# Kernel optimization log

Hardware: AMD Instinct MI355X
Metric: run time of the kernel (lower is better)

Reference implementation:

```python
import jax, jax.numpy as jnp
import numpy as np

NUM_GROUP, GROUP_SIZE = 128, 32
MASK = (64, 32, 32)
FEAT_DIM, N_POINTS = 1024, 2048
NBR_K = int(1.2 * GROUP_SIZE)  # int(nbr_ratio * group_size) = 38
SUPPORT, NBHD = 8, 32
W_RECON, W_MATCH, W_LATENT, W_MAN = 1.0, 1.0, 1.0, 0.1

gather = jax.vmap(lambda p, i: p[i])  # batched index_points

def sqdist(a, b):  # [B,M,3],[B,N,3] -> [B,M,N]
    return (jnp.sum(a * a, -1)[:, :, None] + jnp.sum(b * b, -1)[:, None, :]
            - 2.0 * jnp.einsum('bmd,bnd->bmn', a, b))

def knn_idx(q, db, k):  # indices into db of k nearest to each query
    return jax.lax.top_k(-sqdist(q, db), k)[1]

def fps(pts, G):  # farthest point sampling, [B,N,3] -> [B,G] indices
    b, n, _ = pts.shape
    def step(carry, _):
        min_d, far = carry
        cur = jnp.take_along_axis(pts, far[:, None, None], axis=1)
        min_d = jnp.minimum(min_d, jnp.sum((pts - cur) ** 2, -1))
        return (min_d, jnp.argmax(min_d, -1).astype(jnp.int32)), far
    init = (jnp.full((b, n), 1e10, dtype=pts.dtype), jnp.zeros((b,), jnp.int32))
    _, idxs = jax.lax.scan(step, init, None, length=G)
    return idxs.T

def bn(h, g, b_, m, v):  # BatchNorm1d, eval-mode running stats
    return (h - m) * jax.lax.rsqrt(v + 1e-5) * g + b_

def chamfer_l1(a, b):
    d = sqdist(a, b)
    d1 = jnp.sqrt(jnp.maximum(jnp.min(d, axis=2), 1e-12))
    d2 = jnp.sqrt(jnp.maximum(jnp.min(d, axis=1), 1e-12))
    return 0.5 * (d1.mean() + d2.mean())

def estimate_normals(xyz, K):  # PCA normal per point + direction disambiguation
    nb = gather(xyz, knn_idx(xyz, xyz, K))          # [B,N,K,3]
    c = nb - nb.mean(axis=2, keepdims=True)
    cov = jnp.einsum('bnki,bnkj->bnij', c, c) / K   # [B,N,3,3]
    _, v = jnp.linalg.eigh(cov)
    n = v[..., 0]                                   # smallest-eigenvalue eigvec
    proj = jnp.einsum('bnkd,bnd->bn', nb - xyz[:, :, None, :], n)
    return n * jnp.where(proj >= 0.0, 1.0, -1.0)[..., None]

def forward_all(pts, W1, b1, g1, be1, m1, v1, W2, b2, W3, b3, g2, be2, m2, v2,
                W4, b4, D1W, D1b, D2W, D2b, D3W, D3b, D4W, D4b):
    bsz = pts.shape[0]
    def encoder(x):  # PCN encoder: pointwise convs + global max pooling
        n = x.shape[1]
        h = jax.nn.relu(bn(x @ W1.T + b1, g1, be1, m1, v1))
        h = h @ W2.T + b2                           # [B,n,256]
        gmax = h.max(axis=1)
        h = jnp.concatenate([jnp.broadcast_to(gmax[:, None, :], (bsz, n, gmax.shape[-1])), h], axis=-1)
        h = jax.nn.relu(bn(h @ W3.T + b3, g2, be2, m2, v2))
        return (h @ W4.T + b4).max(axis=1)          # [B,FEAT_DIM]
    def decoder(z):
        h = jax.nn.relu(z @ D1W.T + D1b)
        h = jax.nn.relu(h @ D2W.T + D2b)
        h = jax.nn.relu(h @ D3W.T + D3b)
        return (h @ D4W.T + D4b).reshape(bsz, -1, 3)
    # --- Group divider: FPS centers + knn neighborhoods (centered) ---
    center = gather(pts, fps(pts, NUM_GROUP))       # [B,G,3]
    nbrs = gather(pts, knn_idx(center, pts, GROUP_SIZE)) - center[:, :, None, :]
    o1, o2 = MASK[0], MASK[0] + MASK[1]             # identity perm partition
    ng = (nbrs[:, :o1], nbrs[:, o1:o2], nbrs[:, o2:])
    cg = (center[:, :o1], center[:, o1:o2], center[:, o2:])
    rebuild0 = (ng[0] + cg[0][:, :, None, :]).reshape(bsz, -1, 3)
    feat = encoder(rebuild0)
    pred = decoder(feat)                            # [B,N_POINTS,3]
    # shape reconstruction loss
    idx = knn_idx(cg[0], pred, NBR_K)
    l_recon = W_RECON * chamfer_l1(rebuild0, gather(pred, idx).reshape(bsz, -1, 3))
    # shape matching loss
    rebuild1 = (ng[1] + cg[1][:, :, None, :]).reshape(bsz, -1, 3)
    idx = knn_idx(cg[1], pred, NBR_K)
    l_match = W_MATCH * chamfer_l1(rebuild1, gather(pred, idx).reshape(bsz, -1, 3))
    # latent reconstruction (detached input) - SmoothL1
    idx = knn_idx(cg[2], pred, GROUP_SIZE)
    feat_recon = encoder(jax.lax.stop_gradient(gather(pred, idx).reshape(bsz, -1, 3)))
    diff = feat - feat_recon
    ad = jnp.abs(diff)
    l_latent = W_LATENT * jnp.where(ad < 1.0, 0.5 * diff * diff, ad - 0.5).mean()
    # manifoldness (normal consistency) constraint
    normals = estimate_normals(pred, NBHD)
    nb = gather(normals, knn_idx(pred, pred, SUPPORT))  # [B,N,8,3]
    a = nb[:, :, :1, :]
    cos = jnp.sum(a * nb, -1) / (jnp.maximum(jnp.linalg.norm(a, axis=-1), 1e-6)
                                 * jnp.maximum(jnp.linalg.norm(nb, axis=-1), 1e-6))
    l_man = W_MAN * jnp.std(1.0 - cos, axis=-1, ddof=1).mean(axis=-1).mean()
    total = l_recon + l_match + l_latent + l_man
    return total, l_recon, l_match, l_latent, l_man


def setup_inputs() -> dict:
    ks = jax.random.split(jax.random.key(0), 10)
    rn = lambda k, sh: jax.random.normal(k, sh, jnp.float32) * 0.02
    z, o = jnp.zeros, jnp.ones
    return dict(
        pts=jax.random.normal(ks[0], (16, 2048, 3), jnp.float32),
        W1=rn(ks[1], (128, 3)), b1=z(128), g1=o(128), be1=z(128), m1=z(128), v1=o(128),
        W2=rn(ks[2], (256, 128)), b2=z(256),
        W3=rn(ks[3], (512, 512)), b3=z(512), g2=o(512), be2=z(512), m2=z(512), v2=o(512),
        W4=rn(ks[4], (FEAT_DIM, 512)), b4=z(FEAT_DIM),
        D1W=rn(ks[5], (2048, FEAT_DIM)), D1b=z(2048),
        D2W=rn(ks[6], (2048, 2048)), D2b=z(2048),
        D3W=rn(ks[7], (2048, 2048)), D3b=z(2048),
        D4W=rn(ks[8], (3 * N_POINTS, 2048)), D4b=z(3 * N_POINTS),
    )


def reference(pts, W1, b1, g1, be1, m1, v1, W2, b2, W3, b3, g2, be2, m2, v2,
              W4, b4, D1W, D1b, D2W, D2b, D3W, D3b, D4W, D4b):
    return forward_all(pts, W1, b1, g1, be1, m1, v1, W2, b2, W3, b3, g2, be2,
                       m2, v2, W4, b4, D1W, D1b, D2W, D2b, D3W, D3b, D4W, D4b)
```

## Files before the change

### kernel.cpp

```cpp
#include <hip/hip_runtime.h>
#include <math.h>

#define BSZ 16
#define NPTS 2048
#define NG 128
#define GS 32
#define NBRK 38

typedef _Float16 f16;
typedef _Float16 f16x8 __attribute__((ext_vector_type(8)));
typedef float f32x4 __attribute__((ext_vector_type(4)));

__device__ __forceinline__ unsigned fkey(float x) {
    unsigned u = __float_as_uint(x);
    return (u >> 31) ? ~u : (u | 0x80000000u);
}
__device__ __forceinline__ float fkey_inv(unsigned k) {
    unsigned u = (k >> 31) ? (k ^ 0x80000000u) : ~k;
    return __uint_as_float(u);
}

__device__ __forceinline__ unsigned wave_min_u32(unsigned v) {
    unsigned t;
    t = (unsigned)__builtin_amdgcn_update_dpp(-1, (int)v, 0x111, 0xF, 0xF, false);
    v = v < t ? v : t;
    t = (unsigned)__builtin_amdgcn_update_dpp(-1, (int)v, 0x112, 0xF, 0xF, false);
    v = v < t ? v : t;
    t = (unsigned)__builtin_amdgcn_update_dpp(-1, (int)v, 0x114, 0xF, 0xF, false);
    v = v < t ? v : t;
    t = (unsigned)__builtin_amdgcn_update_dpp(-1, (int)v, 0x118, 0xF, 0xF, false);
    v = v < t ? v : t;
    t = (unsigned)__builtin_amdgcn_update_dpp(-1, (int)v, 0x142, 0xA, 0xF, false);
    v = v < t ? v : t;
    t = (unsigned)__builtin_amdgcn_update_dpp(-1, (int)v, 0x143, 0xC, 0xF, false);
    v = v < t ? v : t;
    return (unsigned)__builtin_amdgcn_readlane((int)v, 63);
}

__device__ __forceinline__ unsigned long long wave_max_u64(unsigned long long v) {
#define DPPSTEP(ctrl, rmask)                                                                \
    {                                                                                       \
        unsigned tlo = (unsigned)__builtin_amdgcn_update_dpp(0, (int)(unsigned)v, ctrl,     \
                                                             rmask, 0xF, false);            \
        unsigned thi = (unsigned)__builtin_amdgcn_update_dpp(0, (int)(unsigned)(v >> 32),   \
                                                             ctrl, rmask, 0xF, false);      \
        unsigned long long t = ((unsigned long long)thi << 32) | tlo;                       \
        v = t > v ? t : v;                                                                  \
    }
    DPPSTEP(0x111, 0xF)
    DPPSTEP(0x112, 0xF)
    DPPSTEP(0x114, 0xF)
    DPPSTEP(0x118, 0xF)
    DPPSTEP(0x142, 0xA)
    DPPSTEP(0x143, 0xC)
#undef DPPSTEP
    unsigned rlo = (unsigned)__builtin_amdgcn_readlane((int)(unsigned)v, 63);
    unsigned rhi = (unsigned)__builtin_amdgcn_readlane((int)(unsigned)(v >> 32), 63);
    return ((unsigned long long)rhi << 32) | rlo;
}

__global__ __launch_bounds__(256, 1) void fps_kernel_v5(const float* __restrict__ pts,
                                                        f32x4* __restrict__ center4) {
    int b = blockIdx.x;
    const float* P = pts + (size_t)b * NPTS * 3;
    int tid = threadIdx.x;
    int lane = tid & 63, wave = tid >> 6;
    __shared__ __align__(16) float Pl[NPTS * 3];
    __shared__ __align__(16) float slot[2][4][8];
#pragma unroll
    for (int i = 0; i < 6; ++i) {
        int v4 = tid + i * 256;
        ((f32x4*)Pl)[v4] = ((const f32x4*)P)[v4];
    }
    __syncthreads();
    float px[8], py[8], pz[8], mind[8];
#pragma unroll
    for (int m = 0; m < 8; ++m) {
        int j = tid + (m << 8);
        px[m] = Pl[j * 3 + 0];
        py[m] = Pl[j * 3 + 1];
        pz[m] = Pl[j * 3 + 2];
        mind[m] = 1e10f;
    }
    float cx = Pl[0], cy = Pl[1], cz = Pl[2];
    f32x4* C4 = center4 + (size_t)b * NG;
#pragma unroll 1
    for (int g = 0; g < NG; ++g) {
        if (tid == 0) C4[g] = (f32x4){cx, cy, cz, cx * cx + cy * cy + cz * cz};
        if (g == NG - 1) break;
        float best0 = -1.f, best1 = -1.f;
        int bm0 = 0, bm1 = 1;
#pragma unroll
        for (int m = 0; m < 8; m += 2) {
            float dx0 = px[m] - cx, dy0 = py[m] - cy, dz0 = pz[m] - cz;
            float d0 = dx0 * dx0 + dy0 * dy0 + dz0 * dz0;
            float md0 = fminf(mind[m], d0);
            mind[m] = md0;
            if (md0 > best0) { best0 = md0; bm0 = m; }
            float dx1 = px[m + 1] - cx, dy1 = py[m + 1] - cy, dz1 = pz[m + 1] - cz;
            float d1 = dx1 * dx1 + dy1 * dy1 + dz1 * dz1;
            float md1 = fminf(mind[m + 1], d1);
            mind[m + 1] = md1;
            if (md1 > best1) { best1 = md1; bm1 = m + 1; }
        }
        bool t = (best1 > best0) || (best1 == best0 && bm1 < bm0);
        float bv = t ? best1 : best0;
        int bi = t ? bm1 : bm0;
        unsigned j = (unsigned)(tid + (bi << 8));
        unsigned long long key =
            ((unsigned long long)__float_as_uint(bv) << 32) | (unsigned)(~j);
        key = wave_max_u64(key);
        unsigned bj = ~(unsigned)key;
        int par = g & 1;
        if (lane < 3) slot[par][wave][2 + lane] = Pl[bj * 3 + lane];
        if (lane == 0) {
            slot[par][wave][0] = __uint_as_float((unsigned)key);
            slot[par][wave][1] = __uint_as_float((unsigned)(key >> 32));
        }
        __syncthreads();
        unsigned long long kb = 0ull;
        float nx = 0.f, ny = 0.f, nz = 0.f;
#pragma unroll
        for (int w = 0; w < 4; ++w) {
            f32x4 v = *(const f32x4*)&slot[par][w][0];
            float vz = slot[par][w][4];
            unsigned long long kk =
                ((unsigned long long)__float_as_uint(v[1]) << 32) | __float_as_uint(v[0]);
            bool tw = kk > kb;
            kb = tw ? kk : kb;
            nx = tw ? v[2] : nx;
            ny = tw ? v[3] : ny;
            nz = tw ? vz : nz;
        }
        cx = nx; cy = ny; cz = nz;
    }
}

__device__ __forceinline__ void knn_query_p4(f32x4 q, const f32x4* __restrict__ db4,
                                             int k, int* __restrict__ o, int lane) {
    const unsigned KINF = 0xFFFFFFFFu;
    float m2x = -2.f * q[0], m2y = -2.f * q[1], m2z = -2.f * q[2], qq = q[3];
    unsigned key[32];
    unsigned c0 = KINF, c1 = KINF, c2 = KINF, c3 = KINF;
#pragma unroll
    for (int m = 0; m < 32; ++m) {
        int j = lane + (m << 6);
        f32x4 b = db4[j];
        float t = fmaf(m2x, b[0], b[3]);
        t = fmaf(m2y, b[1], t);
        t = fmaf(m2z, b[2], t);
        float dv = qq + t;
        unsigned qd = (unsigned)fminf(fmaxf(dv, 0.f) * 8192.0f, 2097151.f);
        unsigned kk = (qd << 11) | (unsigned)j;
        key[m] = kk;
        if (kk < c3) {
            if (kk < c2) {
                c3 = c2;
                if (kk < c1) {
                    c2 = c1;
                    if (kk < c0) { c1 = c0; c0 = kk; } else c1 = kk;
                } else c2 = kk;
            } else c3 = kk;
        }
    }
    unsigned hw = c3;
    int ncached = 4;
    for (int r = 0; r < k; ++r) {
        bool need = (c0 == KINF) && (ncached < 32);
        if (__any(need)) {
            unsigned best = KINF;
#pragma unroll
            for (int m = 0; m < 32; ++m) {
                unsigned v = key[m];
                best = (v > hw && v < best) ? v : best;
            }
            if (need) {
                c0 = best;
                hw = best;
                ncached = (best == KINF) ? 32 : ncached + 1;
            }
        }
        unsigned g = wave_min_u32(c0);
        if (lane == 0) o[r] = (int)(g & 0x7FFu);
        if (((g & 0x7FFu) & 63u) == (unsigned)lane) {
            c0 = c1; c1 = c2; c2 = c3; c3 = KINF;
        }
    }
}

__global__ void knn_group_kernel(const f32x4* __restrict__ center4,
                                 const f32x4* __restrict__ pts4,
                                 int* __restrict__ knnc) {
    int wave = threadIdx.x >> 6, lane = threadIdx.x & 63;
    int qidx = blockIdx.x * 4 + wave;
    int b = qidx >> 7, qi = qidx & 127;
    knn_query_p4(center4[(size_t)b * NG + qi], pts4 + (size_t)b * NPTS, GS,
                 knnc + (size_t)qidx * GS, lane);
}

__global__ void knn_post_kernel(const f32x4* __restrict__ center4,
                                const f32x4* __restrict__ pred4,
                                int* __restrict__ idxa, int* __restrict__ idxb,
                                int* __restrict__ idxc, int* __restrict__ knn32) {
    int wave = threadIdx.x >> 6, lane = threadIdx.x & 63;
    if (blockIdx.x < 512) {
        int qidx = blockIdx.x * 4 + wave;
        int b = qidx >> 7, qi = qidx & 127;
        const f32x4* db4 = pred4 + (size_t)b * NPTS;
        int k; int* o;
        if (qi < 64) { k = NBRK; o = idxa + ((size_t)b * 64 + qi) * NBRK; }
        else if (qi < 96) { k = NBRK; o = idxb + ((size_t)b * 32 + qi - 64) * NBRK; }
        else { k = GS; o = idxc + ((size_t)b * 32 + qi - 96) * GS; }
        knn_query_p4(center4[(size_t)b * NG + qi], db4, k, o, lane);
    } else {
        int qidx = (blockIdx.x - 512) * 4 + wave;
        int b = qidx >> 11, qi = qidx & 2047;
        const f32x4* db4 = pred4 + (size_t)b * NPTS;
        knn_query_p4(db4[qi], db4, GS, knn32 + (size_t)qidx * GS, lane);
    }
}

__global__ void gather_rebuild_kernel(const f32x4* __restrict__ pts4,
                                      const int* __restrict__ knnc,
                                      f32x4* __restrict__ r0p4,
                                      f32x4* __restrict__ r1p4) {
    int t = blockIdx.x * 256 + threadIdx.x;
    if (t < BSZ * 2048) {
        int b = t >> 11, j = t & 2047;
        int s = knnc[(size_t)b * (NG * GS) + j];
        r0p4[t] = pts4[(size_t)b * NPTS + s];
    } else {
        int tt = t - BSZ * 2048;
        int b = tt >> 10, j = tt & 1023;
        int s = knnc[(size_t)b * (NG * GS) + 2048 + j];
        r1p4[tt] = pts4[(size_t)b * NPTS + s];
    }
}

__global__ void gather_abc_kernel(const f32x4* __restrict__ pred4,
                                  const int* __restrict__ idxa,
                                  const int* __restrict__ idxb,
                                  const int* __restrict__ idxc,
                                  f32x4* __restrict__ gap4,
                                  f32x4* __restrict__ gbp4,
                                  f32x4* __restrict__ gathc4) {
    const int NA = BSZ * 2432, NB_ = BSZ * 1216, NC = BSZ * 1024;
    int t = blockIdx.x * 256 + threadIdx.x;
    if (t < NA) {
        int b = t / 2432, j = t - b * 2432;
        int s = idxa[(size_t)b * 2432 + j];
        gap4[t] = pred4[(size_t)b * NPTS + s];
    } else if (t < NA + NB_) {
        int tt = t - NA;
        int b = tt / 1216, j = tt - b * 1216;
        int s = idxb[(size_t)b * 1216 + j];
        gbp4[tt] = pred4[(size_t)b * NPTS + s];
    } else if (t < NA + NB_ + NC) {
        int tt = t - NA - NB_;
        int b = tt >> 10, j = tt & 1023;
        int s = idxc[(size_t)b * 1024 + j];
        gathc4[tt] = pred4[(size_t)b * NPTS + s];
    }
}

__global__ void cvt_all_kernel(const float* __restrict__ W2, const float* __restrict__ W3,
                               const float* __restrict__ W4, const float* __restrict__ pts,
                               f16* __restrict__ W2h, f16* __restrict__ W3h,
                               f16* __restrict__ W4h, f32x4* __restrict__ pts4) {
    int t = blockIdx.x * 256 + threadIdx.x;
    if (t < 32768) {
        int n = t >> 7, k = t & 127;
        W2h[t] = (f16)W2[(size_t)n * 128 + k];
    } else if (t < 163840) {
        int u = t - 32768;
        int n = u >> 8, k = u & 255;
        W3h[u] = (f16)W3[(size_t)n * 512 + 256 + k];
    } else if (t < 688128) {
        int u = t - 163840;
        int n = u >> 9, k = u & 511;
        W4h[u] = (f16)W4[(size_t)n * 512 + k];
    } else if (t < 688128 + BSZ * NPTS) {
        int u = t - 688128;
        float x = pts[(size_t)u * 3 + 0], y = pts[(size_t)u * 3 + 1],
              z = pts[(size_t)u * 3 + 2];
        pts4[u] = (f32x4){x, y, z, x * x + y * y + z * z};
    }
}

__global__ void pack_pred4_kernel(const float* __restrict__ pred,
                                  f32x4* __restrict__ pred4) {
    int t = blockIdx.x * 256 + threadIdx.x;
    if (t >= BSZ * NPTS) return;
    float x = pred[(size_t)t * 3 + 0], y = pred[(size_t)t * 3 + 1],
          z = pred[(size_t)t * 3 + 2];
    pred4[t] = (f32x4){x, y, z, x * x + y * y + z * z};
}

__global__ void layer1_kernel(const f32x4* __restrict__ X4, const float* __restrict__ W1,
                              const float* __restrict__ b1, const float* __restrict__ g1,
                              const float* __restrict__ be1, const float* __restrict__ m1,
                              const float* __restrict__ v1, f16* __restrict__ H1, int M) {
    __shared__ float w[384], bb[128], sg[128], sb[128], sm[128], sv[128];
    for (int i = threadIdx.x; i < 384; i += 256) w[i] = W1[i];
    if (threadIdx.x < 128) {
        int c = threadIdx.x;
        bb[c] = b1[c]; sg[c] = g1[c]; sb[c] = be1[c]; sm[c] = m1[c]; sv[c] = v1[c];
    }
    __syncthreads();
    int t = blockIdx.x * 256 + threadIdx.x;
    if (t >= M * 16) return;
    int row = t >> 4, cg = (t & 15) * 8;
    f32x4 xv = X4[row];
    float x0 = xv[0], x1 = xv[1], x2 = xv[2];
    f16x8 outv;
#pragma unroll
    for (int j = 0; j < 8; ++j) {
        int c = cg + j;
        float tv = x0 * w[c * 3] + x1 * w[c * 3 + 1] + x2 * w[c * 3 + 2] + bb[c];
        float vv = (tv - sm[c]) * rsqrtf(sv[c] + 1e-5f) * sg[c] + sb[c];
        outv[j] = (f16)fmaxf(vv, 0.f);
    }
    *(f16x8*)&H1[(size_t)row * 128 + cg] = outv;
}

__global__ __launch_bounds__(256) void mfma_gemm_kernel(
        const f16* __restrict__ A, const f16* __restrict__ W, int K, int N,
        const float* __restrict__ bias, const float* __restrict__ bias2d,
        const float* __restrict__ bng, const float* __restrict__ bnb,
        const float* __restrict__ bnm, const float* __restrict__ bnv,
        f16* __restrict__ Cout, unsigned* __restrict__ maxkey,
        int rows_per_batch, int relu) {
    __shared__ f16 Als[128 * 40];
    __shared__ f16 Bls[128 * 40];
    int tid = threadIdx.x;
    int lane = tid & 63;
    int wave = tid >> 6;
    int wm = wave & 1, wn = wave >> 1;
    int c16 = lane & 15, quad = lane >> 4;
    int gx = gridDim.x;
    int nwg = gx * gridDim.y;
    int lin = blockIdx.y * gx + blockIdx.x;
    int qc = nwg >> 3, rc = nwg & 7;
    int xcd = lin & 7, pos = lin >> 3;
    int nlin = (xcd < rc ? xcd * (qc + 1) : rc * (qc + 1) + (xcd - rc) * qc) + pos;
    int row0 = (nlin / gx) * 128, col0 = (nlin % gx) * 128;
    int sr = tid >> 2;
    int skc = (tid & 3) * 8;

    f32x4 acc[4][4];
#pragma unroll
    for (int i = 0; i < 4; ++i)
#pragma unroll
        for (int j = 0; j < 4; ++j) acc[i][j] = (f32x4){0.f, 0.f, 0.f, 0.f};

    const f16* Ab = A + (size_t)(row0 + sr) * K + skc;
    const f16* Ab2 = A + (size_t)(row0 + sr + 64) * K + skc;
    const f16* Wb = W + (size_t)(col0 + sr) * K + skc;
    const f16* Wb2 = W + (size_t)(col0 + sr + 64) * K + skc;

    f16x8 pa0 = *(const f16x8*)Ab;
    f16x8 pa1 = *(const f16x8*)Ab2;
    f16x8 pb0 = *(const f16x8*)Wb;
    f16x8 pb1 = *(const f16x8*)Wb2;

    for (int k0 = 0; k0 < K; k0 += 32) {
        *(f16x8*)&Als[sr * 40 + skc] = pa0;
        *(f16x8*)&Als[(sr + 64) * 40 + skc] = pa1;
        *(f16x8*)&Bls[sr * 40 + skc] = pb0;
        *(f16x8*)&Bls[(sr + 64) * 40 + skc] = pb1;
        __syncthreads();
        if (k0 + 32 < K) {
            int kn = k0 + 32;
            pa0 = *(const f16x8*)(Ab + kn);
            pa1 = *(const f16x8*)(Ab2 + kn);
            pb0 = *(const f16x8*)(Wb + kn);
            pb1 = *(const f16x8*)(Wb2 + kn);
        }
        f16x8 af[4], bf[4];
#pragma unroll
        for (int s = 0; s < 4; ++s) {
            af[s] = *(const f16x8*)&Als[(wm * 64 + s * 16 + c16) * 40 + quad * 8];
            bf[s] = *(const f16x8*)&Bls[(wn * 64 + s * 16 + c16) * 40 + quad * 8];
        }
#pragma unroll
        for (int ms = 0; ms < 4; ++ms)
#pragma unroll
            for (int ns = 0; ns < 4; ++ns)
                acc[ms][ns] = __builtin_amdgcn_mfma_f32_16x16x32_f16(af[ms], bf[ns],
                                                                     acc[ms][ns], 0, 0, 0);
        __syncthreads();
    }

    int b = row0 / rows_per_batch;
#pragma unroll
    for (int ns = 0; ns < 4; ++ns) {
        int col = col0 + wn * 64 + ns * 16 + c16;
        float bv = bias ? bias[col] : 0.f;
        float b2v = bias2d ? bias2d[(size_t)b * N + col] : 0.f;
        float mx = -3e38f;
#pragma unroll
        for (int ms = 0; ms < 4; ++ms) {
#pragma unroll
            for (int j = 0; j < 4; ++j) {
                float v = acc[ms][ns][j] + bv + b2v;
                if (bng) v = (v - bnm[col]) * rsqrtf(bnv[col] + 1e-5f) * bng[col] + bnb[col];
                if (relu) v = fmaxf(v, 0.f);
                if (Cout)
                    Cout[(size_t)(row0 + wm * 64 + ms * 16 + quad * 4 + j) * N + col] = (f16)v;
                mx = fmaxf(mx, v);
            }
        }
        if (maxkey) {
            mx = fmaxf(mx, __shfl_xor(mx, 16, 64));
            mx = fmaxf(mx, __shfl_xor(mx, 32, 64));
            if (quad == 0) atomicMax(&maxkey[(size_t)b * N + col], fkey(mx));
        }
    }
}

__global__ void skinny_v2_kernel(const float* __restrict__ A, const float* __restrict__ W,
                                 int ldw, int woff, const float* __restrict__ bias,
                                 float* __restrict__ C, int K, int N, int relu, int akey) {
    int wave = threadIdx.x >> 6, lane = threadIdx.x & 63;
    int col = blockIdx.x * 4 + wave;
    if (col >= N) return;
    const float* w = W + (size_t)col * ldw + woff;
    float acc[16];
#pragma unroll
    for (int m = 0; m < 16; ++m) acc[m] = 0.f;
    for (int k0 = 0; k0 < K; k0 += 256) {
        f32x4 wv = *(const f32x4*)(w + k0 + lane * 4);
#pragma unroll
        for (int m = 0; m < 16; ++m) {
            f32x4 av = *(const f32x4*)(A + (size_t)m * K + k0 + lane * 4);
            if (akey) {
#pragma unroll
                for (int u = 0; u < 4; ++u) av[u] = fkey_inv(__float_as_uint(av[u]));
            }
            acc[m] += av[0] * wv[0] + av[1] * wv[1] + av[2] * wv[2] + av[3] * wv[3];
        }
    }
#pragma unroll
    for (int m = 0; m < 16; ++m)
#pragma unroll
        for (int s = 1; s < 64; s <<= 1) acc[m] += __shfl_xor(acc[m], s, 64);
    if (lane == 0) {
        float bv = bias[col];
#pragma unroll
        for (int m = 0; m < 16; ++m) {
            float v = acc[m] + bv;
            if (relu) v = fmaxf(v, 0.f);
            C[(size_t)m * N + col] = v;
        }
    }
}

__global__ __launch_bounds__(256) void chamfer4_kernel(const f32x4* __restrict__ r0p4,
                                                       const f32x4* __restrict__ gap4,
                                                       const f32x4* __restrict__ r1p4,
                                                       const f32x4* __restrict__ gbp4,
                                                       float* __restrict__ accum) {
    __shared__ __align__(16) float Bl[2432 * 4];
    int blk = blockIdx.x;
    const f32x4 *A4, *B4; int na, nb, base, bpb; float* slot;
    if (blk < 128)      { A4 = r0p4; na = 2048; B4 = gap4; nb = 2432; slot = accum + 0; base = 0;   bpb = 8; }
    else if (blk < 288) { A4 = gap4; na = 2432; B4 = r0p4; nb = 2048; slot = accum + 1; base = 128; bpb = 10; }
    else if (blk < 352) { A4 = r1p4; na = 1024; B4 = gbp4; nb = 1216; slot = accum + 2; base = 288; bpb = 4; }
    else                { A4 = gbp4; na = 1216; B4 = r1p4; nb = 1024; slot = accum + 3; base = 352; bpb = 5; }
    int rel = blk - base;
    int b = rel / bpb, chunk = rel - b * bpb;
    for (int i = threadIdx.x; i < nb; i += 256)
        ((f32x4*)Bl)[i] = B4[(size_t)b * nb + i];
    __syncthreads();
    int aidx = chunk * 256 + threadIdx.x;
    float val = 0.f;
    if (aidx < na) {
        f32x4 a = A4[(size_t)b * na + aidx];
        float m2x = -2.f * a[0], m2y = -2.f * a[1], m2z = -2.f * a[2];
        float m0 = 3e38f, m1 = 3e38f, m2 = 3e38f, m3 = 3e38f;
        for (int j = 0; j < nb; j += 4) {
            f32x4 b0 = ((const f32x4*)Bl)[j + 0];
            f32x4 b1 = ((const f32x4*)Bl)[j + 1];
            f32x4 b2 = ((const f32x4*)Bl)[j + 2];
            f32x4 b3 = ((const f32x4*)Bl)[j + 3];
            float t0 = fmaf(m2z, b0[2], fmaf(m2y, b0[1], fmaf(m2x, b0[0], b0[3])));
            float t1 = fmaf(m2z, b1[2], fmaf(m2y, b1[1], fmaf(m2x, b1[0], b1[3])));
            float t2 = fmaf(m2z, b2[2], fmaf(m2y, b2[1], fmaf(m2x, b2[0], b2[3])));
            float t3 = fmaf(m2z, b3[2], fmaf(m2y, b3[1], fmaf(m2x, b3[0], b3[3])));
            m0 = fminf(m0, t0); m1 = fminf(m1, t1);
            m2 = fminf(m2, t2); m3 = fminf(m3, t3);
        }
        float m = fminf(fminf(m0, m1), fminf(m2, m3));
        val = sqrtf(fmaxf(a[3] + m, 1e-12f));
    }
    __shared__ float sdata[256];
    sdata[threadIdx.x] = val;
    __syncthreads();
    for (int s = 128; s > 0; s >>= 1) {
        if (threadIdx.x < s) sdata[threadIdx.x] += sdata[threadIdx.x + s];
        __syncthreads();
    }
    if (threadIdx.x == 0) atomicAdd(slot, sdata[0]);
}

__device__ void smallest_evec(double cxx, double cxy, double cxz,
                              double cyy, double cyz, double czz, double ev[3]) {
    double p1 = cxy * cxy + cxz * cxz + cyz * cyz;
    double q = (cxx + cyy + czz) / 3.0;
    double p2 = (cxx - q) * (cxx - q) + (cyy - q) * (cyy - q) + (czz - q) * (czz - q) + 2.0 * p1;
    double lam = q;
    if (p2 > 0.0) {
        double p = sqrt(p2 / 6.0);
        double b00 = (cxx - q) / p, b11 = (cyy - q) / p, b22 = (czz - q) / p;
        double b01 = cxy / p, b02 = cxz / p, b12 = cyz / p;
        double detB = b00 * (b11 * b22 - b12 * b12) - b01 * (b01 * b22 - b12 * b02)
                    + b02 * (b01 * b12 - b11 * b02);
        double r = detB * 0.5;
        r = r < -1.0 ? -1.0 : (r > 1.0 ? 1.0 : r);
        double phi = acos(r) / 3.0;
        lam = q + 2.0 * p * cos(phi + 2.0943951023931953);
    }
    double r0x = cxx - lam, r0y = cxy, r0z = cxz;
    double r1x = cxy, r1y = cyy - lam, r1z = cyz;
    double r2x = cxz, r2y = cyz, r2z = czz - lam;
    double c0x = r0y * r1z - r0z * r1y, c0y = r0z * r1x - r0x * r1z, c0z = r0x * r1y - r0y * r1x;
    double c1x = r0y * r2z - r0z * r2y, c1y = r0z * r2x - r0x * r2z, c1z = r0x * r2y - r0y * r2x;
    double c2x = r1y * r2z - r1z * r2y, c2y = r1z * r2x - r1x * r2z, c2z = r1x * r2y - r1y * r2x;
    double n0 = c0x * c0x + c0y * c0y + c0z * c0z;
    double n1 = c1x * c1x + c1y * c1y + c1z * c1z;
    double n2 = c2x * c2x + c2y * c2y + c2z * c2z;
    double bx = c0x, by = c0y, bz = c0z, bn = n0;
    if (n1 > bn) { bx = c1x; by = c1y; bz = c1z; bn = n1; }
    if (n2 > bn) { bx = c2x; by = c2y; bz = c2z; bn = n2; }
    if (bn < 1e-280) { ev[0] = 1.0; ev[1] = 0.0; ev[2] = 0.0; return; }
    double inv = 1.0 / sqrt(bn);
    ev[0] = bx * inv; ev[1] = by * inv; ev[2] = bz * inv;
}

__global__ __launch_bounds__(64) void normals_kernel(const f32x4* __restrict__ pred4,
                                                     const int* __restrict__ knn,
                                                     float* __restrict__ nrm) {
    int t = blockIdx.x * 64 + threadIdx.x;
    if (t >= BSZ * NPTS) return;
    int b = t / NPTS, i = t % NPTS;
    const f32x4* P4 = pred4 + (size_t)b * NPTS;
    const int* id = knn + (size_t)t * 32;
    double sx = 0, sy = 0, sz = 0;
    double sxx = 0, sxy = 0, sxz = 0, syy = 0, syz = 0, szz = 0;
#pragma unroll
    for (int k0 = 0; k0 < 32; k0 += 4) {
        int4 jj = *(const int4*)&id[k0];
#pragma unroll
        for (int u = 0; u < 4; ++u) {
            int j = (u == 0) ? jj.x : (u == 1) ? jj.y : (u == 2) ? jj.z : jj.w;
            f32x4 p = P4[j];
            double x = (double)p[0], y = (double)p[1], z = (double)p[2];
            sx += x; sy += y; sz += z;
            sxx += x * x; sxy += x * y; sxz += x * z;
            syy += y * y; syz += y * z; szz += z * z;
        }
    }
    double mx = sx * (1.0 / 32.0), my = sy * (1.0 / 32.0), mz = sz * (1.0 / 32.0);
    double cxx = sxx * (1.0 / 32.0) - mx * mx;
    double cxy = sxy * (1.0 / 32.0) - mx * my;
    double cxz = sxz * (1.0 / 32.0) - mx * mz;
    double cyy = syy * (1.0 / 32.0) - my * my;
    double cyz = syz * (1.0 / 32.0) - my * mz;
    double czz = szz * (1.0 / 32.0) - mz * mz;
    double ev[3];
    smallest_evec(cxx, cxy, cxz, cyy, cyz, czz, ev);
    f32x4 q = P4[i];
    double proj = (sx - 32.0 * (double)q[0]) * ev[0] + (sy - 32.0 * (double)q[1]) * ev[1]
                + (sz - 32.0 * (double)q[2]) * ev[2];
    double s = (proj >= 0.0) ? 1.0 : -1.0;
    nrm[(size_t)t * 3 + 0] = (float)(ev[0] * s);
    nrm[(size_t)t * 3 + 1] = (float)(ev[1] * s);
    nrm[(size_t)t * 3 + 2] = (float)(ev[2] * s);
}

__global__ void loss_tail_kernel(const float* __restrict__ nrm,
                                 const int* __restrict__ knn32,
                                 const unsigned* __restrict__ k1,
                                 const unsigned* __restrict__ k2,
                                 float* __restrict__ accum) {
    float val = 0.f;
    float* slot;
    if (blockIdx.x < 128) {
        slot = accum + 5;
        int t = blockIdx.x * 256 + threadIdx.x;
        int b = t >> 11;
        const float* NB = nrm + (size_t)b * NPTS * 3;
        const int* id = knn32 + (size_t)t * 32;
        int j0 = id[0];
        float ax = NB[j0 * 3 + 0], ay = NB[j0 * 3 + 1], az = NB[j0 * 3 + 2];
        float an = fmaxf(sqrtf(ax * ax + ay * ay + az * az), 1e-6f);
        float x[8]; float s = 0.f;
        for (int k = 0; k < 8; ++k) {
            int j = id[k];
            float bx = NB[j * 3 + 0], by = NB[j * 3 + 1], bz = NB[j * 3 + 2];
            float bn_ = fmaxf(sqrtf(bx * bx + by * by + bz * bz), 1e-6f);
            float c = (ax * bx + ay * by + az * bz) / (an * bn_);
            x[k] = 1.f - c; s += x[k];
        }
        float mean = s / 8.f;
        float var = 0.f;
        for (int k = 0; k < 8; ++k) { float d = x[k] - mean; var += d * d; }
        val = sqrtf(var / 7.f);
    } else {
        slot = accum + 4;
        int t = (blockIdx.x - 128) * 256 + threadIdx.x;
        float d = fkey_inv(k1[t]) - fkey_inv(k2[t]);
        float ad = fabsf(d);
        val = (ad < 1.f) ? (0.5f * d * d) : (ad - 0.5f);
    }
    __shared__ float sdata[256];
    sdata[threadIdx.x] = val;
    __syncthreads();
    for (int s2 = 128; s2 > 0; s2 >>= 1) {
        if (threadIdx.x < s2) sdata[threadIdx.x] += sdata[threadIdx.x + s2];
        __syncthreads();
    }
    if (threadIdx.x == 0) atomicAdd(slot, sdata[0]);
}

__global__ void finalize_kernel(const float* __restrict__ acc, float* __restrict__ out) {
    float l_recon = 0.5f * (acc[0] / (16.f * 2048.f) + acc[1] / (16.f * 2432.f));
    float l_match = 0.5f * (acc[2] / (16.f * 1024.f) + acc[3] / (16.f * 1216.f));
    float l_latent = acc[4] / (16.f * 1024.f);
    float l_man = 0.1f * (acc[5] / (16.f * 2048.f));
    out[0] = l_recon + l_match + l_latent + l_man;
    out[1] = l_recon;
    out[2] = l_match;
    out[3] = l_latent;
    out[4] = l_man;
}

extern "C" void kernel_launch(void* const* d_in, const int* in_sizes, int n_in,
                              void* d_out, int out_size, void* d_ws, size_t ws_size,
                              hipStream_t stream) {
    (void)in_sizes; (void)n_in; (void)out_size; (void)ws_size;
    const float* pts = (const float*)d_in[0];
    const float* W1 = (const float*)d_in[1];
    const float* b1 = (const float*)d_in[2];
    const float* g1 = (const float*)d_in[3];
    const float* be1 = (const float*)d_in[4];
    const float* m1 = (const float*)d_in[5];
    const float* v1 = (const float*)d_in[6];
    const float* W2 = (const float*)d_in[7];
    const float* b2 = (const float*)d_in[8];
    const float* W3 = (const float*)d_in[9];
    const float* b3 = (const float*)d_in[10];
    const float* g2 = (const float*)d_in[11];
    const float* be2 = (const float*)d_in[12];
    const float* m2 = (const float*)d_in[13];
    const float* v2 = (const float*)d_in[14];
    const float* W4 = (const float*)d_in[15];
    const float* b4 = (const float*)d_in[16];
    const float* D1W = (const float*)d_in[17];
    const float* D1b = (const float*)d_in[18];
    const float* D2W = (const float*)d_in[19];
    const float* D2b = (const float*)d_in[20];
    const float* D3W = (const float*)d_in[21];
    const float* D3b = (const float*)d_in[22];
    const float* D4W = (const float*)d_in[23];
    const float* D4b = (const float*)d_in[24];

    char* ws = (char*)d_ws;
    size_t off = 0;
    auto alloc = [&](size_t bytes) -> void* {
        void* p = ws + off;
        off += (bytes + 255) & ~(size_t)255;
        return p;
    };
    f32x4* center4  = (f32x4*)alloc((size_t)BSZ * NG * 16);
    f32x4* pts4     = (f32x4*)alloc((size_t)BSZ * NPTS * 16);
    f32x4* pred4    = (f32x4*)alloc((size_t)BSZ * NPTS * 16);
    int*   knnc     = (int*)  alloc((size_t)BSZ * NG * GS * 4);
    f32x4* r0p4     = (f32x4*)alloc((size_t)BSZ * 2048 * 16);
    f32x4* r1p4     = (f32x4*)alloc((size_t)BSZ * 1024 * 16);
    f16*   W2h      = (f16*)  alloc((size_t)256 * 128 * 2);
    f16*   W3h      = (f16*)  alloc((size_t)512 * 256 * 2);
    f16*   W4h      = (f16*)  alloc((size_t)1024 * 512 * 2);
    f16*   H1h      = (f16*)  alloc((size_t)BSZ * 2048 * 128 * 2);
    f16*   H2h      = (f16*)  alloc((size_t)BSZ * 2048 * 256 * 2);
    f16*   H3h      = (f16*)  alloc((size_t)BSZ * 2048 * 512 * 2);
    unsigned* keybase = (unsigned*)alloc(((size_t)BSZ * 2560 + 64) * 4);
    unsigned* gmaxkey1 = keybase;
    unsigned* gmaxkey2 = keybase + (size_t)BSZ * 256;
    unsigned* featkey1 = keybase + (size_t)BSZ * 512;
    unsigned* featkey2 = keybase + (size_t)BSZ * 512 + (size_t)BSZ * 1024;
    float* accum = (float*)(keybase + (size_t)BSZ * 2560);
    float* gpart    = (float*)alloc((size_t)BSZ * 512 * 4);
    float* dh1      = (float*)alloc((size_t)BSZ * 2048 * 4);
    float* dh2      = (float*)alloc((size_t)BSZ * 2048 * 4);
    float* dh3      = (float*)alloc((size_t)BSZ * 2048 * 4);
    float* pred     = (float*)alloc((size_t)BSZ * 6144 * 4);
    int*   idxa     = (int*)  alloc((size_t)BSZ * 64 * NBRK * 4);
    int*   idxb     = (int*)  alloc((size_t)BSZ * 32 * NBRK * 4);
    int*   idxc     = (int*)  alloc((size_t)BSZ * 32 * 32 * 4);
    f32x4* gap4     = (f32x4*)alloc((size_t)BSZ * 2432 * 16);
    f32x4* gbp4     = (f32x4*)alloc((size_t)BSZ * 1216 * 16);
    f32x4* gathc4   = (f32x4*)alloc((size_t)BSZ * 1024 * 16);
    int*   knn32    = (int*)  alloc((size_t)BSZ * 2048 * 32 * 4);
    float* nrmbuf   = (float*)alloc((size_t)BSZ * 2048 * 3 * 4);

    hipMemsetAsync(keybase, 0, ((size_t)BSZ * 2560 + 8) * 4, stream);

    cvt_all_kernel<<<2816, 256, 0, stream>>>(W2, W3, W4, pts, W2h, W3h, W4h, pts4);

    fps_kernel_v5<<<BSZ, 256, 0, stream>>>(pts, center4);
    knn_group_kernel<<<(BSZ * NG) / 4, 256, 0, stream>>>(center4, pts4, knnc);
    gather_rebuild_kernel<<<(BSZ * 3072) / 256, 256, 0, stream>>>(pts4, knnc, r0p4, r1p4);

    auto enc = [&](const f32x4* X4, int n, unsigned* gkey, unsigned* fkeyout) {
        int M = BSZ * n;
        layer1_kernel<<<M / 16, 256, 0, stream>>>(X4, W1, b1, g1, be1, m1, v1, H1h, M);
        mfma_gemm_kernel<<<dim3(256 / 128, M / 128), 256, 0, stream>>>(
            H1h, W2h, 128, 256, b2, nullptr, nullptr, nullptr, nullptr, nullptr,
            H2h, gkey, n, 0);
        skinny_v2_kernel<<<(512 + 3) / 4, 256, 0, stream>>>(
            (const float*)gkey, W3, 512, 0, b3, gpart, 256, 512, 0, 1);
        mfma_gemm_kernel<<<dim3(512 / 128, M / 128), 256, 0, stream>>>(
            H2h, W3h, 256, 512, nullptr, gpart, g2, be2, m2, v2, H3h, nullptr, n, 1);
        mfma_gemm_kernel<<<dim3(1024 / 128, M / 128), 256, 0, stream>>>(
            H3h, W4h, 512, 1024, b4, nullptr, nullptr, nullptr, nullptr, nullptr,
            nullptr, fkeyout, n, 0);
    };

    enc(r0p4, 2048, gmaxkey1, featkey1);

    skinny_v2_kernel<<<2048 / 4, 256, 0, stream>>>((const float*)featkey1, D1W, 1024, 0,
                                                   D1b, dh1, 1024, 2048, 1, 1);
    skinny_v2_kernel<<<2048 / 4, 256, 0, stream>>>(dh1, D2W, 2048, 0, D2b, dh2,
                                                   2048, 2048, 1, 0);
    skinny_v2_kernel<<<2048 / 4, 256, 0, stream>>>(dh2, D3W, 2048, 0, D3b, dh3,
                                                   2048, 2048, 1, 0);
    skinny_v2_kernel<<<6144 / 4, 256, 0, stream>>>(dh3, D4W, 2048, 0, D4b, pred,
                                                   2048, 6144, 0, 0);
    pack_pred4_kernel<<<(BSZ * NPTS) / 256, 256, 0, stream>>>(pred, pred4);

    knn_post_kernel<<<512 + (BSZ * NPTS) / 4, 256, 0, stream>>>(center4, pred4, idxa,
                                                                idxb, idxc, knn32);
    gather_abc_kernel<<<(BSZ * 4672) / 256, 256, 0, stream>>>(pred4, idxa, idxb, idxc,
                                                              gap4, gbp4, gathc4);
    chamfer4_kernel<<<432, 256, 0, stream>>>(r0p4, gap4, r1p4, gbp4, accum);
    normals_kernel<<<(BSZ * NPTS) / 64, 64, 0, stream>>>(pred4, knn32, nrmbuf);

    enc(gathc4, 1024, gmaxkey2, featkey2);
    loss_tail_kernel<<<192, 256, 0, stream>>>(nrmbuf, knn32, featkey1, featkey2, accum);

    finalize_kernel<<<1, 1, 0, stream>>>(accum, (float*)d_out);
}
```

Before: 668.8 us.

## Fuse kNN with gathers, pred packing into last GEMM, memset and finalize into kernels

The kNN queries now keep each selected index in a per-lane register and gather the neighbour points directly, which removes the separate gather kernels and their index buffers. The group kNN now runs only the 96 centers whose points are actually used. The last decoder layer gets a dedicated kernel that emits packed xyz plus squared-norm points directly, replacing the generic GEMM and the pack kernel. The memset is folded into the conversion kernel, and finalize moves into the last block of the loss-tail kernel through an atomic ticket. Together these cut several launches and intermediate global-memory round trips, at the cost of a last-block atomic protocol and a specialised pred kernel.

```diff
diff --git a/kernel.cpp b/kernel.cpp
--- a/kernel.cpp
+++ b/kernel.cpp
@@ -136,8 +136,8 @@
     }
 }
 
-__device__ __forceinline__ void knn_query_p4(f32x4 q, const f32x4* __restrict__ db4,
-                                             int k, int* __restrict__ o, int lane) {
+__device__ __forceinline__ int knn_query_core(f32x4 q, const f32x4* __restrict__ db4,
+                                              int k, int lane) {
     const unsigned KINF = 0xFFFFFFFFu;
     float m2x = -2.f * q[0], m2y = -2.f * q[1], m2z = -2.f * q[2], qq = q[3];
     unsigned key[32];
@@ -165,6 +165,7 @@
     }
     unsigned hw = c3;
     int ncached = 4;
+    int mywin = 0;
     for (int r = 0; r < k; ++r) {
         bool need = (c0 == KINF) && (ncached < 32);
         if (__any(need)) {
@@ -181,92 +182,62 @@
             }
         }
         unsigned g = wave_min_u32(c0);
-        if (lane == 0) o[r] = (int)(g & 0x7FFu);
-        if (((g & 0x7FFu) & 63u) == (unsigned)lane) {
+        int idx = (int)(g & 0x7FFu);
+        if (lane == r) mywin = idx;
+        if (((unsigned)idx & 63u) == (unsigned)lane) {
             c0 = c1; c1 = c2; c2 = c3; c3 = KINF;
         }
     }
-}
-
-__global__ void knn_group_kernel(const f32x4* __restrict__ center4,
-                                 const f32x4* __restrict__ pts4,
-                                 int* __restrict__ knnc) {
+    return mywin;
+}
+
+__global__ void knn_group_gather_kernel(const f32x4* __restrict__ center4,
+                                        const f32x4* __restrict__ pts4,
+                                        f32x4* __restrict__ r0p4,
+                                        f32x4* __restrict__ r1p4) {
     int wave = threadIdx.x >> 6, lane = threadIdx.x & 63;
     int qidx = blockIdx.x * 4 + wave;
-    int b = qidx >> 7, qi = qidx & 127;
-    knn_query_p4(center4[(size_t)b * NG + qi], pts4 + (size_t)b * NPTS, GS,
-                 knnc + (size_t)qidx * GS, lane);
+    int b = qidx / 96, qi = qidx - b * 96;
+    const f32x4* db4 = pts4 + (size_t)b * NPTS;
+    int win = knn_query_core(center4[(size_t)b * NG + qi], db4, GS, lane);
+    if (lane < GS) {
+        f32x4 p = db4[win];
+        if (qi < 64) r0p4[(size_t)b * 2048 + qi * GS + lane] = p;
+        else         r1p4[(size_t)b * 1024 + (qi - 64) * GS + lane] = p;
+    }
 }
 
 __global__ void knn_post_kernel(const f32x4* __restrict__ center4,
                                 const f32x4* __restrict__ pred4,
-                                int* __restrict__ idxa, int* __restrict__ idxb,
-                                int* __restrict__ idxc, int* __restrict__ knn32) {
+                                f32x4* __restrict__ gap4, f32x4* __restrict__ gbp4,
+                                f32x4* __restrict__ gathc4, int* __restrict__ knn32) {
     int wave = threadIdx.x >> 6, lane = threadIdx.x & 63;
     if (blockIdx.x < 512) {
         int qidx = blockIdx.x * 4 + wave;
         int b = qidx >> 7, qi = qidx & 127;
         const f32x4* db4 = pred4 + (size_t)b * NPTS;
-        int k; int* o;
-        if (qi < 64) { k = NBRK; o = idxa + ((size_t)b * 64 + qi) * NBRK; }
-        else if (qi < 96) { k = NBRK; o = idxb + ((size_t)b * 32 + qi - 64) * NBRK; }
-        else { k = GS; o = idxc + ((size_t)b * 32 + qi - 96) * GS; }
-        knn_query_p4(center4[(size_t)b * NG + qi], db4, k, o, lane);
+        int k = (qi < 96) ? NBRK : GS;
+        int win = knn_query_core(center4[(size_t)b * NG + qi], db4, k, lane);
+        if (lane < k) {
+            f32x4 p = db4[win];
+            if (qi < 64)      gap4[(size_t)b * 2432 + qi * NBRK + lane] = p;
+            else if (qi < 96) gbp4[(size_t)b * 1216 + (qi - 64) * NBRK + lane] = p;
+            else              gathc4[(size_t)b * 1024 + (qi - 96) * GS + lane] = p;
+        }
     } else {
         int qidx = (blockIdx.x - 512) * 4 + wave;
         int b = qidx >> 11, qi = qidx & 2047;
         const f32x4* db4 = pred4 + (size_t)b * NPTS;
-        knn_query_p4(db4[qi], db4, GS, knn32 + (size_t)qidx * GS, lane);
-    }
-}
-
-__global__ void gather_rebuild_kernel(const f32x4* __restrict__ pts4,
-                                      const int* __restrict__ knnc,
-                                      f32x4* __restrict__ r0p4,
-                                      f32x4* __restrict__ r1p4) {
-    int t = blockIdx.x * 256 + threadIdx.x;
-    if (t < BSZ * 2048) {
-        int b = t >> 11, j = t & 2047;
-        int s = knnc[(size_t)b * (NG * GS) + j];
-        r0p4[t] = pts4[(size_t)b * NPTS + s];
-    } else {
-        int tt = t - BSZ * 2048;
-        int b = tt >> 10, j = tt & 1023;
-        int s = knnc[(size_t)b * (NG * GS) + 2048 + j];
-        r1p4[tt] = pts4[(size_t)b * NPTS + s];
-    }
-}
-
-__global__ void gather_abc_kernel(const f32x4* __restrict__ pred4,
-                                  const int* __restrict__ idxa,
-                                  const int* __restrict__ idxb,
-                                  const int* __restrict__ idxc,
-                                  f32x4* __restrict__ gap4,
-                                  f32x4* __restrict__ gbp4,
-                                  f32x4* __restrict__ gathc4) {
-    const int NA = BSZ * 2432, NB_ = BSZ * 1216, NC = BSZ * 1024;
-    int t = blockIdx.x * 256 + threadIdx.x;
-    if (t < NA) {
-        int b = t / 2432, j = t - b * 2432;
-        int s = idxa[(size_t)b * 2432 + j];
-        gap4[t] = pred4[(size_t)b * NPTS + s];
-    } else if (t < NA + NB_) {
-        int tt = t - NA;
-        int b = tt / 1216, j = tt - b * 1216;
-        int s = idxb[(size_t)b * 1216 + j];
-        gbp4[tt] = pred4[(size_t)b * NPTS + s];
-    } else if (t < NA + NB_ + NC) {
-        int tt = t - NA - NB_;
-        int b = tt >> 10, j = tt & 1023;
-        int s = idxc[(size_t)b * 1024 + j];
-        gathc4[tt] = pred4[(size_t)b * NPTS + s];
+        int win = knn_query_core(db4[qi], db4, GS, lane);
+        if (lane < GS) knn32[(size_t)qidx * GS + lane] = win;
     }
 }
 
 __global__ void cvt_all_kernel(const float* __restrict__ W2, const float* __restrict__ W3,
                                const float* __restrict__ W4, const float* __restrict__ pts,
                                f16* __restrict__ W2h, f16* __restrict__ W3h,
-                               f16* __restrict__ W4h, f32x4* __restrict__ pts4) {
+                               f16* __restrict__ W4h, f32x4* __restrict__ pts4,
+                               unsigned* __restrict__ keybase, int zero_words) {
     int t = blockIdx.x * 256 + threadIdx.x;
     if (t < 32768) {
         int n = t >> 7, k = t & 127;
@@ -279,21 +250,14 @@
         int u = t - 163840;
         int n = u >> 9, k = u & 511;
         W4h[u] = (f16)W4[(size_t)n * 512 + k];
-    } else if (t < 688128 + BSZ * NPTS) {
+    } else if (t < 720896) {
         int u = t - 688128;
         float x = pts[(size_t)u * 3 + 0], y = pts[(size_t)u * 3 + 1],
               z = pts[(size_t)u * 3 + 2];
         pts4[u] = (f32x4){x, y, z, x * x + y * y + z * z};
-    }
-}
-
-__global__ void pack_pred4_kernel(const float* __restrict__ pred,
-                                  f32x4* __restrict__ pred4) {
-    int t = blockIdx.x * 256 + threadIdx.x;
-    if (t >= BSZ * NPTS) return;
-    float x = pred[(size_t)t * 3 + 0], y = pred[(size_t)t * 3 + 1],
-          z = pred[(size_t)t * 3 + 2];
-    pred4[t] = (f32x4){x, y, z, x * x + y * y + z * z};
+    } else if (t < 720896 + zero_words) {
+        keybase[t - 720896] = 0u;
+    }
 }
 
 __global__ void layer1_kernel(const f32x4* __restrict__ X4, const float* __restrict__ W1,
@@ -451,6 +415,48 @@
             float v = acc[m] + bv;
             if (relu) v = fmaxf(v, 0.f);
             C[(size_t)m * N + col] = v;
+        }
+    }
+}
+
+__global__ void skinny_pred3_kernel(const float* __restrict__ A,
+                                    const float* __restrict__ W,
+                                    const float* __restrict__ bias,
+                                    f32x4* __restrict__ pred4) {
+    int wave = threadIdx.x >> 6, lane = threadIdx.x & 63;
+    int p = blockIdx.x * 4 + wave;
+    const float* w0 = W + (size_t)(3 * p + 0) * 2048;
+    const float* w1 = W + (size_t)(3 * p + 1) * 2048;
+    const float* w2 = W + (size_t)(3 * p + 2) * 2048;
+    float ax[16], ay[16], az[16];
+#pragma unroll
+    for (int m = 0; m < 16; ++m) { ax[m] = 0.f; ay[m] = 0.f; az[m] = 0.f; }
+    for (int k0 = 0; k0 < 2048; k0 += 256) {
+        f32x4 wx = *(const f32x4*)(w0 + k0 + lane * 4);
+        f32x4 wy = *(const f32x4*)(w1 + k0 + lane * 4);
+        f32x4 wz = *(const f32x4*)(w2 + k0 + lane * 4);
+#pragma unroll
+        for (int m = 0; m < 16; ++m) {
+            f32x4 av = *(const f32x4*)(A + (size_t)m * 2048 + k0 + lane * 4);
+            ax[m] += av[0] * wx[0] + av[1] * wx[1] + av[2] * wx[2] + av[3] * wx[3];
+            ay[m] += av[0] * wy[0] + av[1] * wy[1] + av[2] * wy[2] + av[3] * wy[3];
+            az[m] += av[0] * wz[0] + av[1] * wz[1] + av[2] * wz[2] + av[3] * wz[3];
+        }
+    }
+#pragma unroll
+    for (int m = 0; m < 16; ++m)
+#pragma unroll
+        for (int s = 1; s < 64; s <<= 1) {
+            ax[m] += __shfl_xor(ax[m], s, 64);
+            ay[m] += __shfl_xor(ay[m], s, 64);
+            az[m] += __shfl_xor(az[m], s, 64);
+        }
+    if (lane == 0) {
+        float bx = bias[3 * p + 0], by = bias[3 * p + 1], bz = bias[3 * p + 2];
+#pragma unroll
+        for (int m = 0; m < 16; ++m) {
+            float x = ax[m] + bx, y = ay[m] + by, z = az[m] + bz;
+            pred4[(size_t)m * 2048 + p] = (f32x4){x, y, z, x * x + y * y + z * z};
         }
     }
 }
@@ -582,7 +588,8 @@
                                  const int* __restrict__ knn32,
                                  const unsigned* __restrict__ k1,
                                  const unsigned* __restrict__ k2,
-                                 float* __restrict__ accum) {
+                                 float* __restrict__ accum,
+                                 float* __restrict__ out) {
     float val = 0.f;
     float* slot;
     if (blockIdx.x < 128) {
@@ -620,19 +627,28 @@
         if (threadIdx.x < s2) sdata[threadIdx.x] += sdata[threadIdx.x + s2];
         __syncthreads();
     }
-    if (threadIdx.x == 0) atomicAdd(slot, sdata[0]);
-}
-
-__global__ void finalize_kernel(const float* __restrict__ acc, float* __restrict__ out) {
-    float l_recon = 0.5f * (acc[0] / (16.f * 2048.f) + acc[1] / (16.f * 2432.f));
-    float l_match = 0.5f * (acc[2] / (16.f * 1024.f) + acc[3] / (16.f * 1216.f));
-    float l_latent = acc[4] / (16.f * 1024.f);
-    float l_man = 0.1f * (acc[5] / (16.f * 2048.f));
-    out[0] = l_recon + l_match + l_latent + l_man;
-    out[1] = l_recon;
-    out[2] = l_match;
-    out[3] = l_latent;
-    out[4] = l_man;
+    if (threadIdx.x == 0) {
+        atomicAdd(slot, sdata[0]);
+        __threadfence();
+        unsigned tk = atomicAdd((unsigned*)(accum + 6), 1u);
+        if (tk == 191u) {
+            float a0 = atomicAdd(&accum[0], 0.f);
+            float a1 = atomicAdd(&accum[1], 0.f);
+            float a2 = atomicAdd(&accum[2], 0.f);
+            float a3 = atomicAdd(&accum[3], 0.f);
+            float a4 = atomicAdd(&accum[4], 0.f);
+            float a5 = atomicAdd(&accum[5], 0.f);
+            float l_recon = 0.5f * (a0 / (16.f * 2048.f) + a1 / (16.f * 2432.f));
+            float l_match = 0.5f * (a2 / (16.f * 1024.f) + a3 / (16.f * 1216.f));
+            float l_latent = a4 / (16.f * 1024.f);
+            float l_man = 0.1f * (a5 / (16.f * 2048.f));
+            out[0] = l_recon + l_match + l_latent + l_man;
+            out[1] = l_recon;
+            out[2] = l_match;
+            out[3] = l_latent;
+            out[4] = l_man;
+        }
+    }
 }
 
 extern "C" void kernel_launch(void* const* d_in, const int* in_sizes, int n_in,
@@ -675,7 +691,6 @@
     f32x4* center4  = (f32x4*)alloc((size_t)BSZ * NG * 16);
     f32x4* pts4     = (f32x4*)alloc((size_t)BSZ * NPTS * 16);
     f32x4* pred4    = (f32x4*)alloc((size_t)BSZ * NPTS * 16);
-    int*   knnc     = (int*)  alloc((size_t)BSZ * NG * GS * 4);
     f32x4* r0p4     = (f32x4*)alloc((size_t)BSZ * 2048 * 16);
     f32x4* r1p4     = (f32x4*)alloc((size_t)BSZ * 1024 * 16);
     f16*   W2h      = (f16*)  alloc((size_t)256 * 128 * 2);
@@ -684,6 +699,7 @@
     f16*   H1h      = (f16*)  alloc((size_t)BSZ * 2048 * 128 * 2);
     f16*   H2h      = (f16*)  alloc((size_t)BSZ * 2048 * 256 * 2);
     f16*   H3h      = (f16*)  alloc((size_t)BSZ * 2048 * 512 * 2);
+    const int kZeroWords = BSZ * 2560 + 16;
     unsigned* keybase = (unsigned*)alloc(((size_t)BSZ * 2560 + 64) * 4);
     unsigned* gmaxkey1 = keybase;
     unsigned* gmaxkey2 = keybase + (size_t)BSZ * 256;
@@ -694,23 +710,18 @@
     float* dh1      = (float*)alloc((size_t)BSZ * 2048 * 4);
     float* dh2      = (float*)alloc((size_t)BSZ * 2048 * 4);
     float* dh3      = (float*)alloc((size_t)BSZ * 2048 * 4);
-    float* pred     = (float*)alloc((size_t)BSZ * 6144 * 4);
-    int*   idxa     = (int*)  alloc((size_t)BSZ * 64 * NBRK * 4);
-    int*   idxb     = (int*)  alloc((size_t)BSZ * 32 * NBRK * 4);
-    int*   idxc     = (int*)  alloc((size_t)BSZ * 32 * 32 * 4);
     f32x4* gap4     = (f32x4*)alloc((size_t)BSZ * 2432 * 16);
     f32x4* gbp4     = (f32x4*)alloc((size_t)BSZ * 1216 * 16);
     f32x4* gathc4   = (f32x4*)alloc((size_t)BSZ * 1024 * 16);
     int*   knn32    = (int*)  alloc((size_t)BSZ * 2048 * 32 * 4);
     float* nrmbuf   = (float*)alloc((size_t)BSZ * 2048 * 3 * 4);
 
-    hipMemsetAsync(keybase, 0, ((size_t)BSZ * 2560 + 8) * 4, stream);
-
-    cvt_all_kernel<<<2816, 256, 0, stream>>>(W2, W3, W4, pts, W2h, W3h, W4h, pts4);
+    cvt_all_kernel<<<(720896 + kZeroWords + 255) / 256, 256, 0, stream>>>(
+        W2, W3, W4, pts, W2h, W3h, W4h, pts4, keybase, kZeroWords);
 
     fps_kernel_v5<<<BSZ, 256, 0, stream>>>(pts, center4);
-    knn_group_kernel<<<(BSZ * NG) / 4, 256, 0, stream>>>(center4, pts4, knnc);
-    gather_rebuild_kernel<<<(BSZ * 3072) / 256, 256, 0, stream>>>(pts4, knnc, r0p4, r1p4);
+    knn_group_gather_kernel<<<(BSZ * 96) / 4, 256, 0, stream>>>(center4, pts4,
+                                                                r0p4, r1p4);
 
     auto enc = [&](const f32x4* X4, int n, unsigned* gkey, unsigned* fkeyout) {
         int M = BSZ * n;
@@ -735,19 +746,15 @@
                                                    2048, 2048, 1, 0);
     skinny_v2_kernel<<<2048 / 4, 256, 0, stream>>>(dh2, D3W, 2048, 0, D3b, dh3,
                                                    2048, 2048, 1, 0);
-    skinny_v2_kernel<<<6144 / 4, 256, 0, stream>>>(dh3, D4W, 2048, 0, D4b, pred,
-                                                   2048, 6144, 0, 0);
-    pack_pred4_kernel<<<(BSZ * NPTS) / 256, 256, 0, stream>>>(pred, pred4);
-
-    knn_post_kernel<<<512 + (BSZ * NPTS) / 4, 256, 0, stream>>>(center4, pred4, idxa,
-                                                                idxb, idxc, knn32);
-    gather_abc_kernel<<<(BSZ * 4672) / 256, 256, 0, stream>>>(pred4, idxa, idxb, idxc,
-                                                              gap4, gbp4, gathc4);
+    skinny_pred3_kernel<<<2048 / 4, 256, 0, stream>>>(dh3, D4W, D4b, pred4);
+
+    knn_post_kernel<<<512 + (BSZ * NPTS) / 4, 256, 0, stream>>>(center4, pred4, gap4,
+                                                                gbp4, gathc4, knn32);
     chamfer4_kernel<<<432, 256, 0, stream>>>(r0p4, gap4, r1p4, gbp4, accum);
     normals_kernel<<<(BSZ * NPTS) / 64, 64, 0, stream>>>(pred4, knn32, nrmbuf);
 
     enc(gathc4, 1024, gmaxkey2, featkey2);
-    loss_tail_kernel<<<192, 256, 0, stream>>>(nrmbuf, knn32, featkey1, featkey2, accum);
-
-    finalize_kernel<<<1, 1, 0, stream>>>(accum, (float*)d_out);
-}
+
+    loss_tail_kernel<<<192, 256, 0, stream>>>(nrmbuf, knn32, featkey1, featkey2,
+                                              accum, (float*)d_out);
+}
```

Measured after the change: 663.5 us. About the same (-0.8%).
